# Performance work log

Hardware: AMD Instinct MI355X
Metric: run time of the kernel (lower is better)

The kernel has to match this reference:

```python
import jax, jax.numpy as jnp
import numpy as np

B, S, HID = 1, 4096, 2048
NH, NKV, HD = 16, 4, 128
BLK, LOCAL, GNB, STRIDE = 64, 4, 2, 4
ROT = 64  # head_dim * rope_partial_rotary_factor(0.5), already even
SCALE = HD ** -0.5
NEG = -1e9


def _block_select(nb):
    """Static local+global key-block selection per query block (mirrors _select_key_blocks)."""
    sels = []
    for bi in range(nb):
        local = list(range(max(0, bi - LOCAL + 1), bi + 1))
        gc = list(range(0, bi + 1, STRIDE))
        if len(gc) > GNB:
            gc = gc[-GNB:]
        if 0 not in gc:
            gc = [0] + gc
        idx = sorted(set(local + gc))
        sels.append([i for i in idx if 0 <= i < nb and i <= bi])
    m = max(len(s) for s in sels)
    idx = np.zeros((nb, m), np.int32)
    valid = np.zeros((nb, m), bool)
    for i, s in enumerate(sels):
        idx[i, :len(s)] = s
        valid[i, :len(s)] = True
    return jnp.asarray(idx), jnp.asarray(valid)


def _rot_half(x):
    h = x.shape[-1] // 2
    return jnp.concatenate([-x[..., h:], x[..., :h]], axis=-1)


def setup_inputs() -> dict:
    key = jax.random.key(0)
    ks = jax.random.split(key, 8)
    w = lambda k, shp: (jax.random.normal(k, shp, jnp.float32) * 0.02)
    return {
        "hidden": jax.random.normal(ks[0], (B, S, HID), jnp.float32),
        "cos": jax.random.uniform(ks[1], (B, S, ROT), jnp.float32, -1.0, 1.0),
        "sin": jax.random.uniform(ks[2], (B, S, ROT), jnp.float32, -1.0, 1.0),
        "Wq": w(ks[3], (HID, NH * HD)),
        "Wk": w(ks[4], (HID, NKV * HD)),
        "Wv": w(ks[5], (HID, NKV * HD)),
        "Wo": w(ks[6], (NH * HD, HID)),
        "attn_mask": jnp.ones((B, S), jnp.float32),
    }


def reference(hidden, cos, sin, Wq, Wk, Wv, Wo, attn_mask):
    b_, s_, _ = hidden.shape
    q = (hidden @ Wq).reshape(b_, s_, NH, HD).transpose(0, 2, 1, 3)   # [B,H,S,d]
    k = (hidden @ Wk).reshape(b_, s_, NKV, HD).transpose(0, 2, 1, 3)  # [B,Hkv,S,d]
    v = (hidden @ Wv).reshape(b_, s_, NKV, HD).transpose(0, 2, 1, 3)

    # partial RoPE on first ROT channels
    c = cos[:, None, :, :]
    sn = sin[:, None, :, :]
    q1, q2 = q[..., :ROT], q[..., ROT:]
    k1, k2 = k[..., :ROT], k[..., ROT:]
    q = jnp.concatenate([q1 * c + _rot_half(q1) * sn, q2], axis=-1)
    k = jnp.concatenate([k1 * c + _rot_half(k1) * sn, k2], axis=-1)

    # repeat_kv (GQA expand: each kv head repeated contiguously)
    rep = NH // NKV
    k = jnp.repeat(k, rep, axis=1)
    v = jnp.repeat(v, rep, axis=1)

    nb = s_ // BLK  # S chosen divisible by BLK (pad_len == 0)
    qb = q.reshape(b_, NH, nb, BLK, HD)
    kb = k.reshape(b_, NH, nb, BLK, HD)
    vb = v.reshape(b_, NH, nb, BLK, HD)

    idx, valid = _block_select(nb)  # [nb, M]
    m = idx.shape[1]
    ksel = kb[:, :, idx]  # [B,H,nb,M,BLK,d]
    vsel = vb[:, :, idx]

    scores = jnp.einsum('bhnqd,bhnmkd->bhnqmk',
                        qb.astype(jnp.float32), ksel.astype(jnp.float32)) * SCALE
    # key-validity (padding) mask, additive as in original
    key_valid = attn_mask.reshape(b_, nb, BLK)
    kvm = key_valid[:, idx]  # [B,nb,M,BLK]
    scores = scores + (1.0 - kvm[:, None, :, None, :, :]) * NEG
    # invalid (padded) selected slots
    scores = jnp.where(valid[None, None, :, None, :, None], scores, NEG)
    # intra-block causal mask on the diagonal block
    intra = jnp.triu(jnp.ones((BLK, BLK), bool), 1)                    # [q,k]
    same = idx == jnp.arange(nb)[:, None]                              # [nb,M]
    diag = same[:, None, :, None] & intra[None, :, None, :]            # [nb,q,M,k]
    scores = jnp.where(diag[None, None], NEG, scores)

    probs = jax.nn.softmax(scores.reshape(b_, NH, nb, BLK, m * BLK), axis=-1)
    vflat = vsel.reshape(b_, NH, nb, m * BLK, HD)
    out = jnp.einsum('bhnqe,bhned->bhnqd', probs.astype(v.dtype), vflat)
    out = out.reshape(b_, NH, s_, HD).transpose(0, 2, 1, 3).reshape(b_, s_, NH * HD)
    return out @ Wo
```

## Files before the change

### kernel.cpp

```cpp
#include <hip/hip_runtime.h>
#include <hip/hip_bf16.h>


typedef short short8 __attribute__((ext_vector_type(8)));
typedef float f32x4  __attribute__((ext_vector_type(4)));

#define NEGV   (-1.0e9f)
#define SCALE  (0.08838834764831845f)

__device__ __forceinline__ void gload16(const void* g, void* l) {
  __builtin_amdgcn_global_load_lds(
      (const __attribute__((address_space(1))) unsigned int*)g,
      (__attribute__((address_space(3))) unsigned int*)l, 16, 0, 0);
}

__device__ __forceinline__ float bf2f(short s) {
  union { unsigned u; float f; } c;
  c.u = ((unsigned)(unsigned short)s) << 16;
  return c.f;
}

__device__ __forceinline__ short f2bf_s(float f) {
  __hip_bfloat16 b = __float2bfloat16(f);
  short s;
  __builtin_memcpy(&s, &b, 2);
  return s;
}

__global__ void conv_hidden(const float* __restrict__ H, __hip_bfloat16* __restrict__ X) {
  size_t t = (size_t)blockIdx.x * 256 + threadIdx.x;
  float4 v = *(const float4*)(H + t * 4);
  __hip_bfloat16* o = X + t * 4;
  o[0] = __float2bfloat16(v.x); o[1] = __float2bfloat16(v.y);
  o[2] = __float2bfloat16(v.z); o[3] = __float2bfloat16(v.w);
}

__global__ void transpose_f32_to_bf16(const float* __restrict__ src,
                                      __hip_bfloat16* __restrict__ dst,
                                      int R, int C) {
  __shared__ __hip_bfloat16 tile[64][73];
  int r0 = blockIdx.x * 64, c0 = blockIdx.y * 64;
  int c = threadIdx.x & 63, rq = threadIdx.x >> 6;
#pragma unroll
  for (int i = 0; i < 16; ++i) {
    int r = i * 4 + rq;
    tile[r][c] = __float2bfloat16(src[(size_t)(r0 + r) * C + c0 + c]);
  }
  __syncthreads();
#pragma unroll
  for (int i = 0; i < 16; ++i) {
    int cc = i * 4 + rq;
    dst[(size_t)(c0 + cc) * R + r0 + c] = tile[c][cc];
  }
}

__global__ void transpose_v(const __hip_bfloat16* __restrict__ Vb,
                            __hip_bfloat16* __restrict__ Vt) {
  __shared__ __hip_bfloat16 tile[64][73];
  int s0 = blockIdx.x * 64, c0 = blockIdx.y * 64;
  int c = threadIdx.x & 63, rq = threadIdx.x >> 6;
#pragma unroll
  for (int i = 0; i < 16; ++i) {
    int r = i * 4 + rq;
    tile[r][c] = Vb[(size_t)(s0 + r) * 512 + c0 + c];
  }
  __syncthreads();
#pragma unroll
  for (int i = 0; i < 16; ++i) {
    int cc = i * 4 + rq;
    Vt[(size_t)(c0 + cc) * 4096 + s0 + c] = tile[c][cc];
  }
}

__global__ void rope_inplace(const float* __restrict__ cosb, const float* __restrict__ sinb,
                             __hip_bfloat16* __restrict__ Qb, __hip_bfloat16* __restrict__ Kb) {
  int t = blockIdx.x * 256 + threadIdx.x;
  __hip_bfloat16* p;
  int s;
  if (t < 262144) {
    s = t >> 6;
    int rem = t & 63;
    p = Qb + (size_t)s * 2048 + (rem >> 2) * 128 + (rem & 3) * 8;
  } else {
    int tk = t - 262144;
    s = tk >> 4;
    int rem = tk & 15;
    p = Kb + (size_t)s * 512 + (rem >> 2) * 128 + (rem & 3) * 8;
  }
  const int g8 = (t & 3) * 8;
  const float* cp = cosb + (size_t)s * 64 + g8;
  const float* sp = sinb + (size_t)s * 64 + g8;
  short8 a = *(const short8*)p;
  short8 b = *(const short8*)(p + 32);
  float ca[8], sa[8], cb[8], sb[8];
  *(float4*)&ca[0] = *(const float4*)cp;        *(float4*)&ca[4] = *(const float4*)(cp + 4);
  *(float4*)&cb[0] = *(const float4*)(cp + 32); *(float4*)&cb[4] = *(const float4*)(cp + 36);
  *(float4*)&sa[0] = *(const float4*)sp;        *(float4*)&sa[4] = *(const float4*)(sp + 4);
  *(float4*)&sb[0] = *(const float4*)(sp + 32); *(float4*)&sb[4] = *(const float4*)(sp + 36);
  short8 oa, ob;
#pragma unroll
  for (int i = 0; i < 8; ++i) {
    float av = bf2f(a[i]), bv = bf2f(b[i]);
    oa[i] = f2bf_s(av * ca[i] - bv * sa[i]);
    ob[i] = f2bf_s(bv * cb[i] + av * sb[i]);
  }
  *(short8*)p = oa;
  *(short8*)(p + 32) = ob;
}

__global__ __launch_bounds__(512, 2) void gemm_qkv8p(
    const __hip_bfloat16* __restrict__ A, const __hip_bfloat16* __restrict__ Bt,
    __hip_bfloat16* __restrict__ Qb, __hip_bfloat16* __restrict__ Kb,
    __hip_bfloat16* __restrict__ Vb) {
  const int K = 2048;
  const int tid = threadIdx.x;
  const int wave = tid >> 6, lane = tid & 63;
  const int l15 = lane & 15, lg = lane >> 4;
  const int bm = blockIdx.x, bn = blockIdx.y;
  const int wm = wave >> 2, wn = wave & 3;

  __shared__ __hip_bfloat16 lds[65536];

  f32x4 acc[8][4] = {};
  const int srow = lane >> 3;
  const int sslot = lane & 7;
  const int scol = (sslot ^ srow) * 8;
  const size_t abase = (size_t)bm * 256 * K;
  const size_t bbase = (size_t)bn * 256 * K;
  const int r3 = l15 & 7;

#define STAGE_HALF(SRC, SBASE, HALF, KO, LBASE)                                  \
  do {                                                                           \
    _Pragma("unroll")                                                            \
    for (int l = 0; l < 2; ++l) {                                                \
      int chunk = l * 8 + wave;                                                  \
      int row = chunk * 8 + srow;                                                \
      gload16(SRC + (SBASE) + (size_t)((HALF) * 128 + row) * K + (KO) + scol,    \
              &lds[(LBASE) + chunk * 512]);                                      \
    }                                                                            \
  } while (0)

  STAGE_HALF(Bt, bbase, 0, 0, 16384);
  STAGE_HALF(Bt, bbase, 1, 0, 16384 + 8192);
  STAGE_HALF(A, abase, 0, 0, 0);
  STAGE_HALF(A, abase, 1, 0, 8192);
  STAGE_HALF(Bt, bbase, 0, 64, 32768 + 16384);
  STAGE_HALF(Bt, bbase, 1, 64, 32768 + 16384 + 8192);
  asm volatile("s_waitcnt vmcnt(4)" ::: "memory");
  __builtin_amdgcn_sched_barrier(0);
  __builtin_amdgcn_s_barrier();

  for (int t = 0; t < 32; ++t) {
    const int buf = (t & 1) * 32768;
    const int nbuf = buf ^ 32768;
    const int bA = buf + wm * 8192;
    const int bB = buf + 16384 + (wn >> 1) * 8192;
    short8 bfr[4][2];
#pragma unroll
    for (int q = 0; q < 4; ++q) {
      if (q == 0) {
#pragma unroll
        for (int ni = 0; ni < 4; ++ni)
#pragma unroll
          for (int ks = 0; ks < 2; ++ks) {
            int row = (wn & 1) * 64 + ni * 16 + l15;
            int slot = (ks * 4 + lg) ^ r3;
            bfr[ni][ks] = *(const short8*)&lds[bB + row * 64 + slot * 8];
          }
      }
      short8 af[2][2];
#pragma unroll
      for (int m2 = 0; m2 < 2; ++m2)
#pragma unroll
        for (int ks = 0; ks < 2; ++ks) {
          int row = (q * 2 + m2) * 16 + l15;
          int slot = (ks * 4 + lg) ^ r3;
          af[m2][ks] = *(const short8*)&lds[bA + row * 64 + slot * 8];
        }
      if (q == 0)      { if (t + 1 < 32) STAGE_HALF(A, abase, 0, (t + 1) * 64, nbuf); }
      else if (q == 1) { if (t + 1 < 32) STAGE_HALF(A, abase, 1, (t + 1) * 64, nbuf + 8192); }
      else if (q == 2) { if (t + 2 < 32) STAGE_HALF(Bt, bbase, 0, (t + 2) * 64, buf + 16384); }
      else {
        if (t + 2 < 32) STAGE_HALF(Bt, bbase, 1, (t + 2) * 64, buf + 16384 + 8192);
        if (t < 30) asm volatile("s_waitcnt vmcnt(4)" ::: "memory");
        else        asm volatile("s_waitcnt vmcnt(0)" ::: "memory");
        __builtin_amdgcn_sched_barrier(0);
      }
      __builtin_amdgcn_s_barrier();
      asm volatile("s_waitcnt lgkmcnt(0)" ::: "memory");
      __builtin_amdgcn_sched_barrier(0);
      __builtin_amdgcn_s_setprio(1);
#pragma unroll
      for (int ks = 0; ks < 2; ++ks)
#pragma unroll
        for (int m2 = 0; m2 < 2; ++m2)
#pragma unroll
          for (int ni = 0; ni < 4; ++ni)
            acc[q * 2 + m2][ni] = __builtin_amdgcn_mfma_f32_16x16x32_bf16(
                af[m2][ks], bfr[ni][ks], acc[q * 2 + m2][ni], 0, 0, 0);
      __builtin_amdgcn_s_setprio(0);
      __builtin_amdgcn_s_barrier();
    }
  }
#undef STAGE_HALF

  __hip_bfloat16* dst; int ldc, coff;
  if (bn < 8)       { dst = Qb; ldc = 2048; coff = bn * 256; }
  else if (bn < 10) { dst = Kb; ldc = 512;  coff = bn * 256 - 2048; }
  else              { dst = Vb; ldc = 512;  coff = bn * 256 - 2560; }
#pragma unroll
  for (int m8 = 0; m8 < 8; ++m8)
#pragma unroll
    for (int ni = 0; ni < 4; ++ni) {
      int row = bm * 256 + wm * 128 + m8 * 16 + lg * 4;
      int col = coff + wn * 64 + ni * 16 + l15;
#pragma unroll
      for (int r = 0; r < 4; ++r)
        dst[(size_t)(row + r) * ldc + col] = __float2bfloat16(acc[m8][ni][r]);
    }
}

__global__ __launch_bounds__(256) void gemm_bt(
    const __hip_bfloat16* __restrict__ A, const __hip_bfloat16* __restrict__ Bt,
    float* __restrict__ C, int M, int N, int K) {
  const int tid = threadIdx.x;
  const int wave = tid >> 6, lane = tid & 63;
  const int l15 = lane & 15, lg = lane >> 4;
  const int bm = blockIdx.x, bn = blockIdx.y;
  const int wm = wave >> 1, wn = wave & 1;

  __shared__ __hip_bfloat16 As[128 * 64];
  __shared__ __hip_bfloat16 Bs[128 * 64];

  f32x4 acc[4][4] = {};
  const int lrow = lane >> 3;
  const int lslot = lane & 7;
  const int scol = (lslot ^ lrow) * 8;
  const size_t abase = (size_t)bm * 128 * K;
  const size_t bbase = (size_t)bn * 128 * K;
  const int r3 = l15 & 7;

  for (int k0 = 0; k0 < K; k0 += 64) {
#pragma unroll
    for (int i = 0; i < 4; ++i) {
      int seg = i * 4 + wave;
      int row = seg * 8 + lrow;
      gload16(A + abase + (size_t)row * K + k0 + scol, &As[seg * 512]);
      gload16(Bt + bbase + (size_t)row * K + k0 + scol, &Bs[seg * 512]);
    }
    __syncthreads();
#pragma unroll
    for (int ks = 0; ks < 2; ++ks) {
      const int slot = (ks * 4 + lg) ^ r3;
      short8 af[4], bf[4];
#pragma unroll
      for (int mi = 0; mi < 4; ++mi)
        af[mi] = *(const short8*)&As[(wm * 64 + mi * 16 + l15) * 64 + slot * 8];
#pragma unroll
      for (int ni = 0; ni < 4; ++ni)
        bf[ni] = *(const short8*)&Bs[(wn * 64 + ni * 16 + l15) * 64 + slot * 8];
#pragma unroll
      for (int mi = 0; mi < 4; ++mi)
#pragma unroll
        for (int ni = 0; ni < 4; ++ni)
          acc[mi][ni] = __builtin_amdgcn_mfma_f32_16x16x32_bf16(af[mi], bf[ni], acc[mi][ni], 0, 0, 0);
    }
    __syncthreads();
  }
#pragma unroll
  for (int mi = 0; mi < 4; ++mi)
#pragma unroll
    for (int ni = 0; ni < 4; ++ni) {
      int row = bm * 128 + wm * 64 + mi * 16 + lg * 4;
      int col = bn * 128 + wn * 64 + ni * 16 + l15;
#pragma unroll
      for (int r = 0; r < 4; ++r)
        C[(size_t)(row + r) * N + col] = acc[mi][ni][r];
    }
}

__global__ __launch_bounds__(256, 2) void attn_kernel(
    const __hip_bfloat16* __restrict__ Qb,
    const __hip_bfloat16* __restrict__ Kb,
    const __hip_bfloat16* __restrict__ Vt,
    const float* __restrict__ amask,
    __hip_bfloat16* __restrict__ AO)
{
  const int bid = blockIdx.x;
  const int h = bid & 15;
  const int bi = bid >> 4;
  const int kvh = h >> 2;
  const int tid = threadIdx.x;
  const int wave = tid >> 6, lane = tid & 63;
  const int l15 = lane & 15, lg = lane >> 4;

  int sel[6]; int nsel = 0;
  {
    int gtop = bi >> 2;
    for (int j = 0; j <= bi; ++j) {
      bool pick = (j == 0) || (j >= bi - 3) || (((j & 3) == 0) && ((j >> 2) >= gtop - 1));
      if (pick && nsel < 6) sel[nsel++] = j;
    }
  }

  __shared__ __hip_bfloat16 kvs[128 * 72];
  __shared__ __hip_bfloat16 Pb[64 * 72];

  short8 qf[4];
  {
    const __hip_bfloat16* qbase =
        Qb + (size_t)(bi * 64 + wave * 16 + l15) * 2048 + h * 128 + lg * 8;
#pragma unroll
    for (int ks = 0; ks < 4; ++ks) qf[ks] = *(const short8*)(qbase + ks * 32);
  }

  f32x4 sc[6][4] = {};
#pragma unroll
  for (int j = 0; j < 6; ++j) {
    if (j < nsel) {
      int kb = sel[j];
#pragma unroll
      for (int i = 0; i < 4; ++i) {
        int e = (i * 256 + tid) * 8;
        int r = e >> 7, c = e & 127;
        short8 v = *(const short8*)(Kb + (size_t)(kb * 64 + r) * 512 + kvh * 128 + c);
        *(short8*)&kvs[r * 136 + c] = v;
      }
      __syncthreads();
#pragma unroll
      for (int nf = 0; nf < 4; ++nf)
#pragma unroll
        for (int ks = 0; ks < 4; ++ks) {
          short8 bfr = *(const short8*)&kvs[(nf * 16 + l15) * 136 + ks * 32 + lg * 8];
          sc[j][nf] = __builtin_amdgcn_mfma_f32_16x16x32_bf16(qf[ks], bfr, sc[j][nf], 0, 0, 0);
        }
      __syncthreads();
    }
  }

  float rowmax[4] = {-3.0e38f, -3.0e38f, -3.0e38f, -3.0e38f};
#pragma unroll
  for (int j = 0; j < 6; ++j) {
    if (j >= nsel) continue;
    int kb = sel[j];
#pragma unroll
    for (int nf = 0; nf < 4; ++nf) {
      int keyg = kb * 64 + nf * 16 + l15;
      float mterm = (1.0f - amask[keyg]) * NEGV;
      int keyl = nf * 16 + l15;
#pragma unroll
      for (int r = 0; r < 4; ++r) {
        float s = sc[j][nf][r] * SCALE + mterm;
        if (kb == bi) {
          int qrow = wave * 16 + lg * 4 + r;
          if (keyl > qrow) s = NEGV;
        }
        sc[j][nf][r] = s;
        rowmax[r] = fmaxf(rowmax[r], s);
      }
    }
  }
#pragma unroll
  for (int r = 0; r < 4; ++r) {
    float v = rowmax[r];
    v = fmaxf(v, __shfl_xor(v, 1)); v = fmaxf(v, __shfl_xor(v, 2));
    v = fmaxf(v, __shfl_xor(v, 4)); v = fmaxf(v, __shfl_xor(v, 8));
    rowmax[r] = v;
  }
  float rinv[4] = {0.f, 0.f, 0.f, 0.f};
#pragma unroll
  for (int j = 0; j < 6; ++j) {
    if (j >= nsel) continue;
#pragma unroll
    for (int nf = 0; nf < 4; ++nf)
#pragma unroll
      for (int r = 0; r < 4; ++r) {
        float p = __expf(sc[j][nf][r] - rowmax[r]);
        sc[j][nf][r] = p;
        rinv[r] += p;
      }
  }
#pragma unroll
  for (int r = 0; r < 4; ++r) {
    float v = rinv[r];
    v += __shfl_xor(v, 1); v += __shfl_xor(v, 2);
    v += __shfl_xor(v, 4); v += __shfl_xor(v, 8);
    rinv[r] = 1.0f / v;
  }

  f32x4 oacc[8] = {};
#pragma unroll
  for (int j = 0; j < 6; ++j) {
    if (j < nsel) {
      int kb = sel[j];
#pragma unroll
      for (int nf = 0; nf < 4; ++nf)
#pragma unroll
        for (int r = 0; r < 4; ++r) {
          int qrow = wave * 16 + lg * 4 + r;
          Pb[qrow * 72 + nf * 16 + l15] = __float2bfloat16(sc[j][nf][r] * rinv[r]);
        }
#pragma unroll
      for (int i = 0; i < 4; ++i) {
        int e = (i * 256 + tid) * 8;
        int d = e >> 6, c = e & 63;
        short8 v = *(const short8*)(Vt + (size_t)(kvh * 128 + d) * 4096 + kb * 64 + c);
        *(short8*)&kvs[d * 72 + c] = v;
      }
      __syncthreads();
#pragma unroll
      for (int ks = 0; ks < 2; ++ks) {
        short8 pa = *(const short8*)&Pb[(wave * 16 + l15) * 72 + ks * 32 + lg * 8];
#pragma unroll
        for (int df = 0; df < 8; ++df) {
          short8 vb = *(const short8*)&kvs[(df * 16 + l15) * 72 + ks * 32 + lg * 8];
          oacc[df] = __builtin_amdgcn_mfma_f32_16x16x32_bf16(pa, vb, oacc[df], 0, 0, 0);
        }
      }
      __syncthreads();
    }
  }

#pragma unroll
  for (int df = 0; df < 8; ++df)
#pragma unroll
    for (int r = 0; r < 4; ++r) {
      int qrow = bi * 64 + wave * 16 + lg * 4 + r;
      AO[(size_t)qrow * 2048 + h * 128 + df * 16 + l15] = __float2bfloat16(oacc[df][r]);
    }
}

extern "C" void kernel_launch(void* const* d_in, const int* in_sizes, int n_in,
                              void* d_out, int out_size, void* d_ws, size_t ws_size,
                              hipStream_t stream) {
  const float* hidden = (const float*)d_in[0];
  const float* cosb   = (const float*)d_in[1];
  const float* sinb   = (const float*)d_in[2];
  const float* Wq     = (const float*)d_in[3];
  const float* Wk     = (const float*)d_in[4];
  const float* Wv     = (const float*)d_in[5];
  const float* Wo     = (const float*)d_in[6];
  const float* amask  = (const float*)d_in[7];

  char* ws = (char*)d_ws;
  __hip_bfloat16* Xb   = (__hip_bfloat16*)(ws);
  __hip_bfloat16* Wt   = (__hip_bfloat16*)(ws + 16777216);
  __hip_bfloat16* Wot  = (__hip_bfloat16*)(ws + 29360128);
  __hip_bfloat16* Qb   = (__hip_bfloat16*)(ws + 37748736);
  __hip_bfloat16* Kb   = (__hip_bfloat16*)(ws + 54525952);
  __hip_bfloat16* Vb   = (__hip_bfloat16*)(ws + 58720256);
  __hip_bfloat16* Vt   = (__hip_bfloat16*)(ws + 62914560);
  __hip_bfloat16* AO   = Xb;

  conv_hidden<<<8192, 256, 0, stream>>>(hidden, Xb);
  transpose_f32_to_bf16<<<dim3(32, 32), 256, 0, stream>>>(Wq, Wt, 2048, 2048);
  transpose_f32_to_bf16<<<dim3(32, 8),  256, 0, stream>>>(Wk, Wt + (size_t)2048 * 2048, 2048, 512);
  transpose_f32_to_bf16<<<dim3(32, 8),  256, 0, stream>>>(Wv, Wt + (size_t)2560 * 2048, 2048, 512);
  transpose_f32_to_bf16<<<dim3(32, 32), 256, 0, stream>>>(Wo, Wot, 2048, 2048);

  gemm_qkv8p<<<dim3(16, 12), 512, 0, stream>>>(Xb, Wt, Qb, Kb, Vb);

  rope_inplace<<<1280, 256, 0, stream>>>(cosb, sinb, Qb, Kb);
  transpose_v<<<dim3(64, 8), 256, 0, stream>>>(Vb, Vt);

  attn_kernel<<<1024, 256, 0, stream>>>(Qb, Kb, Vt, amask, AO);

  gemm_bt<<<dim3(32, 16), 256, 0, stream>>>(AO, Wot, (float*)d_out, 4096, 2048, 2048);
}
```

Measured before the change: 176.8 us.

## Fuse prep kernels into one launch and software-pipeline LDS fragment reads in QKV GEMM

Merges the hidden conversion and four weight-transpose launches into a single prep_all kernel that dispatches on block index, removing four kernel launches and their gaps. The QKV GEMM main loop is restructured to double-buffer A fragments in registers. Each quarter's LDS reads are issued while the previous quarter's MFMAs run, and the next tile's B/A fragments are prefetched at the end of the iteration. This also drops one barrier per quarter. It adds register pressure under the 512x2 launch bound.

Result: faster. 169.1 us (-4.4%).

```diff
diff --git a/kernel.cpp b/kernel.cpp
--- a/kernel.cpp
+++ b/kernel.cpp
@@ -27,19 +27,26 @@
   return s;
 }
 
-__global__ void conv_hidden(const float* __restrict__ H, __hip_bfloat16* __restrict__ X) {
-  size_t t = (size_t)blockIdx.x * 256 + threadIdx.x;
-  float4 v = *(const float4*)(H + t * 4);
-  __hip_bfloat16* o = X + t * 4;
-  o[0] = __float2bfloat16(v.x); o[1] = __float2bfloat16(v.y);
-  o[2] = __float2bfloat16(v.z); o[3] = __float2bfloat16(v.w);
-}
-
-__global__ void transpose_f32_to_bf16(const float* __restrict__ src,
-                                      __hip_bfloat16* __restrict__ dst,
-                                      int R, int C) {
+__global__ void prep_all(const float* __restrict__ H, const float* __restrict__ Wq,
+                         const float* __restrict__ Wk, const float* __restrict__ Wv,
+                         const float* __restrict__ Wo, __hip_bfloat16* __restrict__ X,
+                         __hip_bfloat16* __restrict__ Wt, __hip_bfloat16* __restrict__ Wot) {
   __shared__ __hip_bfloat16 tile[64][73];
-  int r0 = blockIdx.x * 64, c0 = blockIdx.y * 64;
+  int b = blockIdx.x;
+  if (b < 8192) {
+    size_t t = (size_t)b * 256 + threadIdx.x;
+    float4 v = *(const float4*)(H + t * 4);
+    __hip_bfloat16* o = X + t * 4;
+    o[0] = __float2bfloat16(v.x); o[1] = __float2bfloat16(v.y);
+    o[2] = __float2bfloat16(v.z); o[3] = __float2bfloat16(v.w);
+    return;
+  }
+  const float* src; __hip_bfloat16* dst; int C; int idx;
+  if (b < 9216)      { src = Wq; dst = Wt;                          C = 2048; idx = b - 8192; }
+  else if (b < 9472) { src = Wk; dst = Wt + (size_t)2048 * 2048;    C = 512;  idx = b - 9216; }
+  else if (b < 9728) { src = Wv; dst = Wt + (size_t)2560 * 2048;    C = 512;  idx = b - 9472; }
+  else               { src = Wo; dst = Wot;                         C = 2048; idx = b - 9728; }
+  int r0 = (idx & 31) * 64, c0 = (idx >> 5) * 64;
   int c = threadIdx.x & 63, rq = threadIdx.x >> 6;
 #pragma unroll
   for (int i = 0; i < 16; ++i) {
@@ -50,7 +57,7 @@
 #pragma unroll
   for (int i = 0; i < 16; ++i) {
     int cc = i * 4 + rq;
-    dst[(size_t)(c0 + cc) * R + r0 + c] = tile[c][cc];
+    dst[(size_t)(c0 + cc) * 2048 + r0 + c] = tile[c][cc];
   }
 }
 
@@ -108,7 +115,7 @@
   *(short8*)(p + 32) = ob;
 }
 
-__global__ __launch_bounds__(512, 2) void gemm_qkv8p(
+__global__ __launch_bounds__(512, 2) void gemm_qkv4p(
     const __hip_bfloat16* __restrict__ A, const __hip_bfloat16* __restrict__ Bt,
     __hip_bfloat16* __restrict__ Qb, __hip_bfloat16* __restrict__ Kb,
     __hip_bfloat16* __restrict__ Vb) {
@@ -130,7 +137,7 @@
   const int r3 = l15 & 7;
 
 #define STAGE_HALF(SRC, SBASE, HALF, KO, LBASE)                                  \
-  do {                                                                           \
+  {                                                                              \
     _Pragma("unroll")                                                            \
     for (int l = 0; l < 2; ++l) {                                                \
       int chunk = l * 8 + wave;                                                  \
@@ -138,71 +145,108 @@
       gload16(SRC + (SBASE) + (size_t)((HALF) * 128 + row) * K + (KO) + scol,    \
               &lds[(LBASE) + chunk * 512]);                                      \
     }                                                                            \
-  } while (0)
+  }
+
+  short8 bfr[4][2];
+  short8 af[2][2][2];
+
+#define READ_AF(P, Q, BA)                                                        \
+  {                                                                              \
+    _Pragma("unroll")                                                            \
+    for (int m2 = 0; m2 < 2; ++m2)                                               \
+      _Pragma("unroll")                                                          \
+      for (int ks = 0; ks < 2; ++ks) {                                           \
+        int row = ((Q) * 2 + m2) * 16 + l15;                                     \
+        int slot = (ks * 4 + lg) ^ r3;                                           \
+        af[P][m2][ks] = *(const short8*)&lds[(BA) + row * 64 + slot * 8];        \
+      }                                                                          \
+  }
+
+#define READ_BF(BB)                                                              \
+  {                                                                              \
+    _Pragma("unroll")                                                            \
+    for (int ni = 0; ni < 4; ++ni)                                               \
+      _Pragma("unroll")                                                          \
+      for (int ks = 0; ks < 2; ++ks) {                                           \
+        int row = (wn & 1) * 64 + ni * 16 + l15;                                 \
+        int slot = (ks * 4 + lg) ^ r3;                                           \
+        bfr[ni][ks] = *(const short8*)&lds[(BB) + row * 64 + slot * 8];          \
+      }                                                                          \
+  }
+
+#define MFMA_Q(Q, P)                                                             \
+  {                                                                              \
+    __builtin_amdgcn_s_setprio(1);                                               \
+    _Pragma("unroll")                                                            \
+    for (int ks = 0; ks < 2; ++ks)                                               \
+      _Pragma("unroll")                                                          \
+      for (int m2 = 0; m2 < 2; ++m2)                                             \
+        _Pragma("unroll")                                                        \
+        for (int ni = 0; ni < 4; ++ni)                                           \
+          acc[(Q) * 2 + m2][ni] = __builtin_amdgcn_mfma_f32_16x16x32_bf16(       \
+              af[P][m2][ks], bfr[ni][ks], acc[(Q) * 2 + m2][ni], 0, 0, 0);       \
+    __builtin_amdgcn_s_setprio(0);                                               \
+  }
+
+#define LGKM0()                                                                  \
+  asm volatile("s_waitcnt lgkmcnt(0)" ::: "memory");                             \
+  __builtin_amdgcn_sched_barrier(0);
 
   STAGE_HALF(Bt, bbase, 0, 0, 16384);
-  STAGE_HALF(Bt, bbase, 1, 0, 16384 + 8192);
+  STAGE_HALF(Bt, bbase, 1, 0, 24576);
   STAGE_HALF(A, abase, 0, 0, 0);
   STAGE_HALF(A, abase, 1, 0, 8192);
-  STAGE_HALF(Bt, bbase, 0, 64, 32768 + 16384);
-  STAGE_HALF(Bt, bbase, 1, 64, 32768 + 16384 + 8192);
+  STAGE_HALF(Bt, bbase, 0, 64, 49152);
+  STAGE_HALF(Bt, bbase, 1, 64, 57344);
   asm volatile("s_waitcnt vmcnt(4)" ::: "memory");
   __builtin_amdgcn_sched_barrier(0);
   __builtin_amdgcn_s_barrier();
+  {
+    const int bA0 = wm * 8192;
+    const int bB0 = 16384 + (wn >> 1) * 8192;
+    READ_BF(bB0);
+    READ_AF(0, 0, bA0);
+  }
+  LGKM0();
 
   for (int t = 0; t < 32; ++t) {
     const int buf = (t & 1) * 32768;
     const int nbuf = buf ^ 32768;
     const int bA = buf + wm * 8192;
-    const int bB = buf + 16384 + (wn >> 1) * 8192;
-    short8 bfr[4][2];
-#pragma unroll
-    for (int q = 0; q < 4; ++q) {
-      if (q == 0) {
-#pragma unroll
-        for (int ni = 0; ni < 4; ++ni)
-#pragma unroll
-          for (int ks = 0; ks < 2; ++ks) {
-            int row = (wn & 1) * 64 + ni * 16 + l15;
-            int slot = (ks * 4 + lg) ^ r3;
-            bfr[ni][ks] = *(const short8*)&lds[bB + row * 64 + slot * 8];
-          }
-      }
-      short8 af[2][2];
-#pragma unroll
-      for (int m2 = 0; m2 < 2; ++m2)
-#pragma unroll
-        for (int ks = 0; ks < 2; ++ks) {
-          int row = (q * 2 + m2) * 16 + l15;
-          int slot = (ks * 4 + lg) ^ r3;
-          af[m2][ks] = *(const short8*)&lds[bA + row * 64 + slot * 8];
-        }
-      if (q == 0)      { if (t + 1 < 32) STAGE_HALF(A, abase, 0, (t + 1) * 64, nbuf); }
-      else if (q == 1) { if (t + 1 < 32) STAGE_HALF(A, abase, 1, (t + 1) * 64, nbuf + 8192); }
-      else if (q == 2) { if (t + 2 < 32) STAGE_HALF(Bt, bbase, 0, (t + 2) * 64, buf + 16384); }
-      else {
-        if (t + 2 < 32) STAGE_HALF(Bt, bbase, 1, (t + 2) * 64, buf + 16384 + 8192);
-        if (t < 30) asm volatile("s_waitcnt vmcnt(4)" ::: "memory");
-        else        asm volatile("s_waitcnt vmcnt(0)" ::: "memory");
-        __builtin_amdgcn_sched_barrier(0);
-      }
-      __builtin_amdgcn_s_barrier();
-      asm volatile("s_waitcnt lgkmcnt(0)" ::: "memory");
-      __builtin_amdgcn_sched_barrier(0);
-      __builtin_amdgcn_s_setprio(1);
-#pragma unroll
-      for (int ks = 0; ks < 2; ++ks)
-#pragma unroll
-        for (int m2 = 0; m2 < 2; ++m2)
-#pragma unroll
-          for (int ni = 0; ni < 4; ++ni)
-            acc[q * 2 + m2][ni] = __builtin_amdgcn_mfma_f32_16x16x32_bf16(
-                af[m2][ks], bfr[ni][ks], acc[q * 2 + m2][ni], 0, 0, 0);
-      __builtin_amdgcn_s_setprio(0);
-      __builtin_amdgcn_s_barrier();
-    }
+    if (t + 1 < 32) STAGE_HALF(A, abase, 0, (t + 1) * 64, nbuf);
+    __builtin_amdgcn_s_barrier();
+    MFMA_Q(0, 0);
+    READ_AF(1, 1, bA);
+    LGKM0();
+    if (t + 1 < 32) STAGE_HALF(A, abase, 1, (t + 1) * 64, nbuf + 8192);
+    __builtin_amdgcn_s_barrier();
+    MFMA_Q(1, 1);
+    READ_AF(0, 2, bA);
+    LGKM0();
+    if (t + 2 < 32) STAGE_HALF(Bt, bbase, 0, (t + 2) * 64, buf + 16384);
+    __builtin_amdgcn_s_barrier();
+    MFMA_Q(2, 0);
+    READ_AF(1, 3, bA);
+    LGKM0();
+    if (t + 2 < 32) STAGE_HALF(Bt, bbase, 1, (t + 2) * 64, buf + 24576);
+    if (t < 30) asm volatile("s_waitcnt vmcnt(4)" ::: "memory");
+    else        asm volatile("s_waitcnt vmcnt(0)" ::: "memory");
+    __builtin_amdgcn_sched_barrier(0);
+    __builtin_amdgcn_s_barrier();
+    MFMA_Q(3, 1);
+    if (t + 1 < 32) {
+      const int nbA = nbuf + wm * 8192;
+      const int nbB = nbuf + 16384 + (wn >> 1) * 8192;
+      READ_BF(nbB);
+      READ_AF(0, 0, nbA);
+    }
+    LGKM0();
   }
 #undef STAGE_HALF
+#undef READ_AF
+#undef READ_BF
+#undef MFMA_Q
+#undef LGKM0
 
   __hip_bfloat16* dst; int ldc, coff;
   if (bn < 8)       { dst = Qb; ldc = 2048; coff = bn * 256; }
@@ -452,13 +496,9 @@
   __hip_bfloat16* Vt   = (__hip_bfloat16*)(ws + 62914560);
   __hip_bfloat16* AO   = Xb;
 
-  conv_hidden<<<8192, 256, 0, stream>>>(hidden, Xb);
-  transpose_f32_to_bf16<<<dim3(32, 32), 256, 0, stream>>>(Wq, Wt, 2048, 2048);
-  transpose_f32_to_bf16<<<dim3(32, 8),  256, 0, stream>>>(Wk, Wt + (size_t)2048 * 2048, 2048, 512);
-  transpose_f32_to_bf16<<<dim3(32, 8),  256, 0, stream>>>(Wv, Wt + (size_t)2560 * 2048, 2048, 512);
-  transpose_f32_to_bf16<<<dim3(32, 32), 256, 0, stream>>>(Wo, Wot, 2048, 2048);
-
-  gemm_qkv8p<<<dim3(16, 12), 512, 0, stream>>>(Xb, Wt, Qb, Kb, Vb);
+  prep_all<<<10752, 256, 0, stream>>>(hidden, Wq, Wk, Wv, Wo, Xb, Wt, Wot);
+
+  gemm_qkv4p<<<dim3(16, 12), 512, 0, stream>>>(Xb, Wt, Qb, Kb, Vb);
 
   rope_inplace<<<1280, 256, 0, stream>>>(cosb, sinb, Qb, Kb);
   transpose_v<<<dim3(64, 8), 256, 0, stream>>>(Vb, Vt);
```
